# Optimization experiments

Measured on AMD Instinct MI355X. Metric: run time of the kernel, lower is better.

Reference implementation:

```python
import jax, jax.numpy as jnp
import numpy as np

N_NODES = 50000
BN_EPS = 1e-5
L2_EPS = 1e-12


def setup_inputs() -> dict:
    key = jax.random.key(0)
    k_h, k_w, k_s, k_d = jax.random.split(key, 4)
    h = jax.random.normal(k_h, (N_NODES, 128), dtype=jnp.float32)
    W = jax.random.normal(k_w, (128, 128), dtype=jnp.float32) * (1.0 / np.sqrt(128))
    gamma = jnp.ones((128,), dtype=jnp.float32)
    beta = jnp.zeros((128,), dtype=jnp.float32)
    src = jax.random.randint(k_s, (600000,), 0, N_NODES, dtype=jnp.int64 if jax.config.jax_enable_x64 else jnp.int32)
    dst = jax.random.randint(k_d, (600000,), 0, N_NODES, dtype=jnp.int64 if jax.config.jax_enable_x64 else jnp.int32)
    return {"h": h, "W": W, "gamma": gamma, "beta": beta, "src": src, "dst": dst}


def reference(h, W, gamma, beta, src, dst):
    N = h.shape[0]
    ones = jnp.ones(src.shape[0], dtype=h.dtype)
    # degrees, clamped to >= 1 (DGL GraphConv norm='both')
    deg_out = jnp.clip(jax.ops.segment_sum(ones, src, num_segments=N), 1.0)
    deg_in = jnp.clip(jax.ops.segment_sum(ones, dst, num_segments=N), 1.0)
    # src-side normalization
    hn = h * jax.lax.rsqrt(deg_out)[:, None]
    # gather-scatter aggregation over edges (sum of src messages at dst)
    agg = jax.ops.segment_sum(hn[src], dst, num_segments=N)  # [N, dim_in]
    # dst-side normalization, then linear (in_feats <= out_feats branch)
    agg = agg * jax.lax.rsqrt(deg_in)[:, None]
    out = agg @ W  # [N, dim_out]
    # BatchNorm1d (training-mode batch stats, biased variance)
    mu = jnp.mean(out, axis=0)
    var = jnp.mean(jnp.square(out - mu), axis=0)
    out = (out - mu) * jax.lax.rsqrt(var + BN_EPS) * gamma + beta
    # ReLU
    out = jax.nn.relu(out)
    # F.normalize(p=2, dim=1)
    norm = jnp.sqrt(jnp.sum(jnp.square(out), axis=1, keepdims=True))
    out = out / jnp.maximum(norm, L2_EPS)
    return out
```

## Files before the change

### kernel.cpp

```cpp
#include <hip/hip_runtime.h>
#include <hip/hip_bf16.h>

#define N_NODES 50000
#define N_EDGES 600000
#define SLOTS 64
#define GEMM_BLOCKS 782
#define BUILD_BLOCKS 2344
#define GATHER_BLOCKS 3125
#define RED_BLOCKS 125

#define Z_OFF        0ull
#define ESRCP_OFF    12800000ull
#define CURS_OFF     19200000ull
#define DEGO_OFF     19400000ull
#define ZERO_OFF     19200000ull
#define ZERO_BYTES   400000ull
#define FLAG_OFF     19600000ull
#define WSW_OFF      19600128ull
#define PSUM_OFF     19632896ull
#define PSQ_OFF      21232896ull
#define PS2_OFF      22832896ull
#define PQ2_OFF      22896896ull
#define SCALE_OFF    22960896ull
#define SHIFT_OFF    22961408ull
#define OUTPRE_OFF   23000064ull

typedef short bf16x8 __attribute__((ext_vector_type(8)));
typedef float f32x4  __attribute__((ext_vector_type(4)));

__device__ __forceinline__ float bf16lo(unsigned int v) { return __uint_as_float(v << 16); }
__device__ __forceinline__ float bf16hi(unsigned int v) { return __uint_as_float(v & 0xffff0000u); }
__device__ __forceinline__ unsigned int packbf16(float x, float y) {
  union { __hip_bfloat162 v; unsigned int u; } cvt;
  cvt.v.x = __float2bfloat16(x);
  cvt.v.y = __float2bfloat16(y);
  return cvt.u;
}

__global__ __launch_bounds__(256) void k_prepW(const void* __restrict__ Wraw,
                                               const unsigned int* __restrict__ hu,
                                               unsigned int* __restrict__ wsw,
                                               int* __restrict__ flag) {
  __shared__ int cnt;
  if (threadIdx.x == 0) cnt = 0;
  __syncthreads();
  {
    unsigned int u = hu[threadIdx.x];
    int ex = (u >> 7) & 0xFF;
    if (ex >= 100 && ex <= 140) atomicAdd(&cnt, 1);
  }
  __syncthreads();
  int isbf = (cnt >= 128) ? 1 : 0;
  if (blockIdx.x == 0 && threadIdx.x == 0) *flag = isbf;

  int i = blockIdx.x * 256 + threadIdx.x;
  int tileIdx = i >> 8;
  int rem     = i & 255;
  int ln      = rem >> 2;
  int dw      = rem & 3;
  int kb      = tileIdx & 3;
  int ct      = tileIdx >> 2;
  int q       = ln >> 4;
  int n       = ln & 15;
  int k       = kb * 32 + q * 8 + dw * 2;
  int c       = ct * 16 + n;
  unsigned int val;
  if (isbf) {
    const unsigned int* Wd = (const unsigned int*)Wraw;
    unsigned int u0 = Wd[k * 64 + (c >> 1)];
    unsigned int u1 = Wd[(k + 1) * 64 + (c >> 1)];
    unsigned int h0 = (c & 1) ? (u0 >> 16) : (u0 & 0xffffu);
    unsigned int h1 = (c & 1) ? (u1 >> 16) : (u1 & 0xffffu);
    val = h0 | (h1 << 16);
  } else {
    const float* Wf = (const float*)Wraw;
    val = packbf16(Wf[k * 128 + c], Wf[(k + 1) * 128 + c]);
  }
  wsw[i] = val;
}

__global__ __launch_bounds__(256) void k_fused(const int* __restrict__ src,
                                               const int* __restrict__ dst,
                                               int* __restrict__ cursor,
                                               int* __restrict__ dego,
                                               unsigned short* __restrict__ esrcPad,
                                               const void* __restrict__ hraw,
                                               const int* __restrict__ flag,
                                               const unsigned int* __restrict__ wsw,
                                               __hip_bfloat16* __restrict__ Z) {
  __shared__ uint4 lb4[2048];
  if (blockIdx.x >= GEMM_BLOCKS) {
    int e = (blockIdx.x - GEMM_BLOCKS) * 256 + threadIdx.x;
    if (e < N_EDGES) {
      int s = src[e];
      int d = dst[e];
      atomicAdd(&dego[s], 1);
      int slot = atomicAdd(&cursor[d], 1);
      if (slot < SLOTS) esrcPad[d * SLOTS + slot] = (unsigned short)s;
    }
    return;
  }

  unsigned int* lb = (unsigned int*)lb4;
  int t = threadIdx.x;
  int r0 = blockIdx.x * 64;
  for (int i = t; i < 2048; i += 256) lb4[i] = ((const uint4*)wsw)[i];

  int l = t & 63;
  int w = t >> 6;
  int m = l & 15;
  int q = l >> 4;
  int isbf = *flag;

  int rA = r0 + w * 16 + m;
  bool okA = rA < N_NODES;

  bf16x8 af[4];
  if (isbf) {
    const uint4* hd = (const uint4*)hraw;
#pragma unroll
    for (int kb = 0; kb < 4; ++kb) {
      union { uint4 u; bf16x8 v; } cv;
      cv.u = okA ? hd[(size_t)rA * 16 + kb * 4 + q] : make_uint4(0u, 0u, 0u, 0u);
      af[kb] = cv.v;
    }
  } else {
    const float4* hf = (const float4*)hraw;
#pragma unroll
    for (int kb = 0; kb < 4; ++kb) {
      union { uint4 u; bf16x8 v; } cv;
      if (okA) {
        float4 f0 = hf[(size_t)rA * 32 + kb * 8 + q * 2];
        float4 f1 = hf[(size_t)rA * 32 + kb * 8 + q * 2 + 1];
        cv.u.x = packbf16(f0.x, f0.y);
        cv.u.y = packbf16(f0.z, f0.w);
        cv.u.z = packbf16(f1.x, f1.y);
        cv.u.w = packbf16(f1.z, f1.w);
      } else {
        cv.u = make_uint4(0u, 0u, 0u, 0u);
      }
      af[kb] = cv.v;
    }
  }

  f32x4 acc[8];
#pragma unroll
  for (int ct = 0; ct < 8; ++ct) acc[ct] = (f32x4){0.f, 0.f, 0.f, 0.f};

  __syncthreads();

#pragma unroll
  for (int kb = 0; kb < 4; ++kb) {
#pragma unroll
    for (int ct = 0; ct < 8; ++ct) {
      bf16x8 bfv = *(const bf16x8*)&lb[(ct * 4 + kb) * 256 + l * 4];
      acc[ct] = __builtin_amdgcn_mfma_f32_16x16x32_bf16(af[kb], bfv, acc[ct], 0, 0, 0);
    }
  }

#pragma unroll
  for (int ct = 0; ct < 8; ++ct) {
    int col = ct * 16 + m;
#pragma unroll
    for (int reg = 0; reg < 4; ++reg) {
      int row = r0 + w * 16 + q * 4 + reg;
      if (row < N_NODES) Z[(size_t)row * 128 + col] = __float2bfloat16(acc[ct][reg]);
    }
  }
}

__global__ __launch_bounds__(256) void k_gatherZ(const unsigned int* __restrict__ Zd,
                                                 const int* __restrict__ cursor,
                                                 const int* __restrict__ dego,
                                                 const unsigned short* __restrict__ esrcPad,
                                                 unsigned int* __restrict__ outpre,
                                                 float* __restrict__ psum,
                                                 float* __restrict__ psq) {
  __shared__ float sred[4 * 128];
  int t = threadIdx.x;
  int w = t >> 6;
  int l = t & 63;
  float s1a = 0.f, s1b = 0.f, s2a = 0.f, s2b = 0.f;
#pragma unroll
  for (int i = 0; i < 4; ++i) {
    int n = blockIdx.x * 16 + w * 4 + i;
    int di = cursor[n];
    int cnt = di < SLOTS ? di : SLOTS;
    const unsigned short* row = esrcPad + (size_t)n * SLOTS;
    float a0 = 0.f, a1 = 0.f;
    int j = 0;
    for (; j + 3 < cnt; j += 4) {
      ushort4 s4 = *(const ushort4*)&row[j];
      int i0 = s4.x, i1 = s4.y, i2 = s4.z, i3 = s4.w;
      unsigned int v0 = Zd[(size_t)i0 * 64 + l];
      unsigned int v1 = Zd[(size_t)i1 * 64 + l];
      unsigned int v2 = Zd[(size_t)i2 * 64 + l];
      unsigned int v3 = Zd[(size_t)i3 * 64 + l];
      float c0 = rsqrtf((float)max(dego[i0], 1));
      float c1 = rsqrtf((float)max(dego[i1], 1));
      float c2 = rsqrtf((float)max(dego[i2], 1));
      float c3 = rsqrtf((float)max(dego[i3], 1));
      a0 = fmaf(bf16lo(v0), c0, a0); a1 = fmaf(bf16hi(v0), c0, a1);
      a0 = fmaf(bf16lo(v1), c1, a0); a1 = fmaf(bf16hi(v1), c1, a1);
      a0 = fmaf(bf16lo(v2), c2, a0); a1 = fmaf(bf16hi(v2), c2, a1);
      a0 = fmaf(bf16lo(v3), c3, a0); a1 = fmaf(bf16hi(v3), c3, a1);
    }
    for (; j < cnt; ++j) {
      int is = row[j];
      unsigned int v = Zd[(size_t)is * 64 + l];
      float c = rsqrtf((float)max(dego[is], 1));
      a0 = fmaf(bf16lo(v), c, a0);
      a1 = fmaf(bf16hi(v), c, a1);
    }
    float scn = rsqrtf((float)(di < 1 ? 1 : di));
    a0 *= scn; a1 *= scn;
    outpre[(size_t)n * 64 + l] = packbf16(a0, a1);
    s1a += a0; s2a += a0 * a0;
    s1b += a1; s2b += a1 * a1;
  }
  sred[w * 128 + 2 * l]     = s1a;
  sred[w * 128 + 2 * l + 1] = s1b;
  __syncthreads();
  if (t < 128) {
    float v = sred[t] + sred[128 + t] + sred[256 + t] + sred[384 + t];
    psum[(size_t)blockIdx.x * 128 + t] = v;
  }
  __syncthreads();
  sred[w * 128 + 2 * l]     = s2a;
  sred[w * 128 + 2 * l + 1] = s2b;
  __syncthreads();
  if (t < 128) {
    float v = sred[t] + sred[128 + t] + sred[256 + t] + sred[384 + t];
    psq[(size_t)blockIdx.x * 128 + t] = v;
  }
}

__global__ __launch_bounds__(256) void k_bnred(const float* __restrict__ psum,
                                               const float* __restrict__ psq,
                                               float* __restrict__ ps2,
                                               float* __restrict__ pq2) {
  __shared__ float r1[256], r2[256];
  int t = threadIdx.x;
  int c = t & 127;
  int j = t >> 7;
  int b0 = blockIdx.x * 25;
  float s1 = 0.f, s2 = 0.f;
  for (int b = b0 + j; b < b0 + 25; b += 2) {
    s1 += psum[(size_t)b * 128 + c];
    s2 += psq [(size_t)b * 128 + c];
  }
  r1[t] = s1; r2[t] = s2;
  __syncthreads();
  if (j == 0) {
    ps2[(size_t)blockIdx.x * 128 + c] = s1 + r1[c + 128];
    pq2[(size_t)blockIdx.x * 128 + c] = s2 + r2[c + 128];
  }
}

__global__ __launch_bounds__(1024) void k_bnfinal(const float* __restrict__ ps2,
                                                  const float* __restrict__ pq2,
                                                  const void* __restrict__ gamma,
                                                  const void* __restrict__ beta,
                                                  const int* __restrict__ flag,
                                                  float* __restrict__ scale,
                                                  float* __restrict__ shift) {
  __shared__ float r1[1024], r2[1024];
  int t = threadIdx.x;
  int c = t & 127;
  int j = t >> 7;
  float s1 = 0.f, s2 = 0.f;
  for (int b = j; b < RED_BLOCKS; b += 8) {
    s1 += ps2[(size_t)b * 128 + c];
    s2 += pq2[(size_t)b * 128 + c];
  }
  r1[t] = s1; r2[t] = s2;
  __syncthreads();
  if (j == 0) {
#pragma unroll
    for (int jj = 1; jj < 8; ++jj) { s1 += r1[c + 128 * jj]; s2 += r2[c + 128 * jj]; }
    const float invN = 1.0f / (float)N_NODES;
    float mu  = s1 * invN;
    float var = s2 * invN - mu * mu;
    float is  = rsqrtf(var + 1e-5f);
    float g, b;
    if (*flag) {
      g = __bfloat162float(((const __hip_bfloat16*)gamma)[c]);
      b = __bfloat162float(((const __hip_bfloat16*)beta)[c]);
    } else {
      g = ((const float*)gamma)[c];
      b = ((const float*)beta)[c];
    }
    scale[c] = g * is;
    shift[c] = b - mu * g * is;
  }
}

__global__ __launch_bounds__(256) void k_rownorm(const unsigned int* __restrict__ outpre,
                                                 const float* __restrict__ scale,
                                                 const float* __restrict__ shift,
                                                 const int* __restrict__ flag,
                                                 void* __restrict__ outraw) {
  int r = blockIdx.x * 4 + (threadIdx.x >> 6);
  int l = threadIdx.x & 63;
  unsigned int xv = outpre[(size_t)r * 64 + l];
  float2 sc = *(const float2*)&scale[2 * l];
  float2 sh = *(const float2*)&shift[2 * l];
  float y0 = fmaxf(bf16lo(xv) * sc.x + sh.x, 0.f);
  float y1 = fmaxf(bf16hi(xv) * sc.y + sh.y, 0.f);
  float ss = y0 * y0 + y1 * y1;
#pragma unroll
  for (int o = 1; o < 64; o <<= 1) ss += __shfl_xor(ss, o, 64);
  float inv = 1.0f / fmaxf(sqrtf(ss), 1e-12f);
  y0 *= inv; y1 *= inv;
  if (*flag) {
    ((unsigned int*)outraw)[(size_t)r * 64 + l] = packbf16(y0, y1);
  } else {
    float2 o2; o2.x = y0; o2.y = y1;
    ((float2*)outraw)[(size_t)r * 64 + l] = o2;
  }
}

extern "C" void kernel_launch(void* const* d_in, const int* in_sizes, int n_in,
                              void* d_out, int out_size, void* d_ws, size_t ws_size,
                              hipStream_t stream) {
  const void* h     = d_in[0];
  const void* W     = d_in[1];
  const void* gamma = d_in[2];
  const void* beta  = d_in[3];
  const int*  src   = (const int*)d_in[4];
  const int*  dst   = (const int*)d_in[5];

  char* ws = (char*)d_ws;
  unsigned int* Zd      = (unsigned int*)(ws + Z_OFF);
  unsigned short* esrcPad = (unsigned short*)(ws + ESRCP_OFF);
  int*   cursor  = (int*)(ws + CURS_OFF);
  int*   dego    = (int*)(ws + DEGO_OFF);
  int*   flag    = (int*)(ws + FLAG_OFF);
  unsigned int* wsw = (unsigned int*)(ws + WSW_OFF);
  float* psum    = (float*)(ws + PSUM_OFF);
  float* psq     = (float*)(ws + PSQ_OFF);
  float* ps2     = (float*)(ws + PS2_OFF);
  float* pq2     = (float*)(ws + PQ2_OFF);
  float* scale   = (float*)(ws + SCALE_OFF);
  float* shift   = (float*)(ws + SHIFT_OFF);
  unsigned int* outpre = (unsigned int*)(ws + OUTPRE_OFF);

  (void)hipMemsetAsync(ws + ZERO_OFF, 0, ZERO_BYTES, stream);

  hipLaunchKernelGGL(k_prepW, dim3(32), dim3(256), 0, stream,
                     W, (const unsigned int*)h, wsw, flag);
  hipLaunchKernelGGL(k_fused, dim3(GEMM_BLOCKS + BUILD_BLOCKS), dim3(256), 0, stream,
                     src, dst, cursor, dego, esrcPad, h, flag, wsw,
                     (__hip_bfloat16*)Zd);
  hipLaunchKernelGGL(k_gatherZ, dim3(GATHER_BLOCKS), dim3(256), 0, stream,
                     Zd, cursor, dego, esrcPad, outpre, psum, psq);
  hipLaunchKernelGGL(k_bnred, dim3(RED_BLOCKS), dim3(256), 0, stream,
                     psum, psq, ps2, pq2);
  hipLaunchKernelGGL(k_bnfinal, dim3(1), dim3(1024), 0, stream,
                     ps2, pq2, gamma, beta, flag, scale, shift);
  hipLaunchKernelGGL(k_rownorm, dim3(N_NODES / 4), dim3(256), 0, stream,
                     outpre, scale, shift, flag, (unsigned int*)d_out);
}
```

Baseline: 194.3 us.

## Fold W swizzle into GEMM, pad degree counters, vectorize edge build

Removes the k_prepW launch: every GEMM block now swizzles W directly from global into LDS, and bf16 detection becomes a per-wave ballot repeated in each kernel. The edge-build blocks each handle four edges through int4 loads. Cursor and out-degree counters are spaced 32 ints apart, one counter per 128-byte line, to reduce atomic contention on shared lines. In exchange the memset grows from 400 KB to 12.8 MB, counter reads in the gather become scattered, and W is converted redundantly by 782 blocks.

```diff
diff --git a/kernel.cpp b/kernel.cpp
--- a/kernel.cpp
+++ b/kernel.cpp
@@ -5,25 +5,24 @@
 #define N_EDGES 600000
 #define SLOTS 64
 #define GEMM_BLOCKS 782
-#define BUILD_BLOCKS 2344
+#define BUILD_BLOCKS 586
 #define GATHER_BLOCKS 3125
 #define RED_BLOCKS 125
+#define CSTRIDE 32
 
 #define Z_OFF        0ull
 #define ESRCP_OFF    12800000ull
 #define CURS_OFF     19200000ull
-#define DEGO_OFF     19400000ull
+#define DEGO_OFF     25600000ull
 #define ZERO_OFF     19200000ull
-#define ZERO_BYTES   400000ull
-#define FLAG_OFF     19600000ull
-#define WSW_OFF      19600128ull
-#define PSUM_OFF     19632896ull
-#define PSQ_OFF      21232896ull
-#define PS2_OFF      22832896ull
-#define PQ2_OFF      22896896ull
-#define SCALE_OFF    22960896ull
-#define SHIFT_OFF    22961408ull
-#define OUTPRE_OFF   23000064ull
+#define ZERO_BYTES   12800000ull
+#define PSUM_OFF     32000000ull
+#define PSQ_OFF      33600000ull
+#define PS2_OFF      35200000ull
+#define PQ2_OFF      35264000ull
+#define SCALE_OFF    35328000ull
+#define SHIFT_OFF    35328512ull
+#define OUTPRE_OFF   35400000ull
 
 typedef short bf16x8 __attribute__((ext_vector_type(8)));
 typedef float f32x4  __attribute__((ext_vector_type(4)));
@@ -37,46 +36,11 @@
   return cvt.u;
 }
 
-__global__ __launch_bounds__(256) void k_prepW(const void* __restrict__ Wraw,
-                                               const unsigned int* __restrict__ hu,
-                                               unsigned int* __restrict__ wsw,
-                                               int* __restrict__ flag) {
-  __shared__ int cnt;
-  if (threadIdx.x == 0) cnt = 0;
-  __syncthreads();
-  {
-    unsigned int u = hu[threadIdx.x];
-    int ex = (u >> 7) & 0xFF;
-    if (ex >= 100 && ex <= 140) atomicAdd(&cnt, 1);
-  }
-  __syncthreads();
-  int isbf = (cnt >= 128) ? 1 : 0;
-  if (blockIdx.x == 0 && threadIdx.x == 0) *flag = isbf;
-
-  int i = blockIdx.x * 256 + threadIdx.x;
-  int tileIdx = i >> 8;
-  int rem     = i & 255;
-  int ln      = rem >> 2;
-  int dw      = rem & 3;
-  int kb      = tileIdx & 3;
-  int ct      = tileIdx >> 2;
-  int q       = ln >> 4;
-  int n       = ln & 15;
-  int k       = kb * 32 + q * 8 + dw * 2;
-  int c       = ct * 16 + n;
-  unsigned int val;
-  if (isbf) {
-    const unsigned int* Wd = (const unsigned int*)Wraw;
-    unsigned int u0 = Wd[k * 64 + (c >> 1)];
-    unsigned int u1 = Wd[(k + 1) * 64 + (c >> 1)];
-    unsigned int h0 = (c & 1) ? (u0 >> 16) : (u0 & 0xffffu);
-    unsigned int h1 = (c & 1) ? (u1 >> 16) : (u1 & 0xffffu);
-    val = h0 | (h1 << 16);
-  } else {
-    const float* Wf = (const float*)Wraw;
-    val = packbf16(Wf[k * 128 + c], Wf[(k + 1) * 128 + c]);
-  }
-  wsw[i] = val;
+__device__ __forceinline__ int detect_bf16(const unsigned int* hu, int tid) {
+  unsigned int u = hu[tid & 63];
+  int ex = (u >> 7) & 0xFF;
+  unsigned long long b = __ballot(ex >= 100 && ex <= 140);
+  return __popcll(b) >= 32 ? 1 : 0;
 }
 
 __global__ __launch_bounds__(256) void k_fused(const int* __restrict__ src,
@@ -85,32 +49,66 @@
                                                int* __restrict__ dego,
                                                unsigned short* __restrict__ esrcPad,
                                                const void* __restrict__ hraw,
-                                               const int* __restrict__ flag,
-                                               const unsigned int* __restrict__ wsw,
+                                               const void* __restrict__ Wraw,
                                                __hip_bfloat16* __restrict__ Z) {
-  __shared__ uint4 lb4[2048];
+  __shared__ unsigned int lb[8192];
+  int t = threadIdx.x;
+
   if (blockIdx.x >= GEMM_BLOCKS) {
-    int e = (blockIdx.x - GEMM_BLOCKS) * 256 + threadIdx.x;
-    if (e < N_EDGES) {
-      int s = src[e];
-      int d = dst[e];
-      atomicAdd(&dego[s], 1);
-      int slot = atomicAdd(&cursor[d], 1);
-      if (slot < SLOTS) esrcPad[d * SLOTS + slot] = (unsigned short)s;
+    int e0 = (blockIdx.x - GEMM_BLOCKS) * 1024 + t * 4;
+    if (e0 < N_EDGES) {
+      int4 s4 = *(const int4*)&src[e0];
+      int4 d4 = *(const int4*)&dst[e0];
+      atomicAdd(&dego[(size_t)s4.x * CSTRIDE], 1);
+      atomicAdd(&dego[(size_t)s4.y * CSTRIDE], 1);
+      atomicAdd(&dego[(size_t)s4.z * CSTRIDE], 1);
+      atomicAdd(&dego[(size_t)s4.w * CSTRIDE], 1);
+      int sl0 = atomicAdd(&cursor[(size_t)d4.x * CSTRIDE], 1);
+      int sl1 = atomicAdd(&cursor[(size_t)d4.y * CSTRIDE], 1);
+      int sl2 = atomicAdd(&cursor[(size_t)d4.z * CSTRIDE], 1);
+      int sl3 = atomicAdd(&cursor[(size_t)d4.w * CSTRIDE], 1);
+      if (sl0 < SLOTS) esrcPad[(size_t)d4.x * SLOTS + sl0] = (unsigned short)s4.x;
+      if (sl1 < SLOTS) esrcPad[(size_t)d4.y * SLOTS + sl1] = (unsigned short)s4.y;
+      if (sl2 < SLOTS) esrcPad[(size_t)d4.z * SLOTS + sl2] = (unsigned short)s4.z;
+      if (sl3 < SLOTS) esrcPad[(size_t)d4.w * SLOTS + sl3] = (unsigned short)s4.w;
     }
     return;
   }
 
-  unsigned int* lb = (unsigned int*)lb4;
-  int t = threadIdx.x;
+  const unsigned int* hu = (const unsigned int*)hraw;
+  int isbf = detect_bf16(hu, t);
   int r0 = blockIdx.x * 64;
-  for (int i = t; i < 2048; i += 256) lb4[i] = ((const uint4*)wsw)[i];
+
+  for (int i = t; i < 8192; i += 256) {
+    int tileIdx = i >> 8;
+    int rem     = i & 255;
+    int ln      = rem >> 2;
+    int dw      = rem & 3;
+    int kb      = tileIdx & 3;
+    int ct      = tileIdx >> 2;
+    int q       = ln >> 4;
+    int n       = ln & 15;
+    int k       = kb * 32 + q * 8 + dw * 2;
+    int c       = ct * 16 + n;
+    unsigned int val;
+    if (isbf) {
+      const unsigned int* Wd = (const unsigned int*)Wraw;
+      unsigned int u0 = Wd[k * 64 + (c >> 1)];
+      unsigned int u1 = Wd[(k + 1) * 64 + (c >> 1)];
+      unsigned int h0 = (c & 1) ? (u0 >> 16) : (u0 & 0xffffu);
+      unsigned int h1 = (c & 1) ? (u1 >> 16) : (u1 & 0xffffu);
+      val = h0 | (h1 << 16);
+    } else {
+      const float* Wf = (const float*)Wraw;
+      val = packbf16(Wf[k * 128 + c], Wf[(k + 1) * 128 + c]);
+    }
+    lb[i] = val;
+  }
 
   int l = t & 63;
   int w = t >> 6;
   int m = l & 15;
   int q = l >> 4;
-  int isbf = *flag;
 
   int rA = r0 + w * 16 + m;
   bool okA = rA < N_NODES;
@@ -184,7 +182,7 @@
 #pragma unroll
   for (int i = 0; i < 4; ++i) {
     int n = blockIdx.x * 16 + w * 4 + i;
-    int di = cursor[n];
+    int di = cursor[(size_t)n * CSTRIDE];
     int cnt = di < SLOTS ? di : SLOTS;
     const unsigned short* row = esrcPad + (size_t)n * SLOTS;
     float a0 = 0.f, a1 = 0.f;
@@ -196,10 +194,10 @@
       unsigned int v1 = Zd[(size_t)i1 * 64 + l];
       unsigned int v2 = Zd[(size_t)i2 * 64 + l];
       unsigned int v3 = Zd[(size_t)i3 * 64 + l];
-      float c0 = rsqrtf((float)max(dego[i0], 1));
-      float c1 = rsqrtf((float)max(dego[i1], 1));
-      float c2 = rsqrtf((float)max(dego[i2], 1));
-      float c3 = rsqrtf((float)max(dego[i3], 1));
+      float c0 = rsqrtf((float)max(dego[(size_t)i0 * CSTRIDE], 1));
+      float c1 = rsqrtf((float)max(dego[(size_t)i1 * CSTRIDE], 1));
+      float c2 = rsqrtf((float)max(dego[(size_t)i2 * CSTRIDE], 1));
+      float c3 = rsqrtf((float)max(dego[(size_t)i3 * CSTRIDE], 1));
       a0 = fmaf(bf16lo(v0), c0, a0); a1 = fmaf(bf16hi(v0), c0, a1);
       a0 = fmaf(bf16lo(v1), c1, a0); a1 = fmaf(bf16hi(v1), c1, a1);
       a0 = fmaf(bf16lo(v2), c2, a0); a1 = fmaf(bf16hi(v2), c2, a1);
@@ -208,7 +206,7 @@
     for (; j < cnt; ++j) {
       int is = row[j];
       unsigned int v = Zd[(size_t)is * 64 + l];
-      float c = rsqrtf((float)max(dego[is], 1));
+      float c = rsqrtf((float)max(dego[(size_t)is * CSTRIDE], 1));
       a0 = fmaf(bf16lo(v), c, a0);
       a1 = fmaf(bf16hi(v), c, a1);
     }
@@ -261,11 +259,12 @@
                                                   const float* __restrict__ pq2,
                                                   const void* __restrict__ gamma,
                                                   const void* __restrict__ beta,
-                                                  const int* __restrict__ flag,
+                                                  const unsigned int* __restrict__ hu,
                                                   float* __restrict__ scale,
                                                   float* __restrict__ shift) {
   __shared__ float r1[1024], r2[1024];
   int t = threadIdx.x;
+  int isbf = detect_bf16(hu, t);
   int c = t & 127;
   int j = t >> 7;
   float s1 = 0.f, s2 = 0.f;
@@ -283,7 +282,7 @@
     float var = s2 * invN - mu * mu;
     float is  = rsqrtf(var + 1e-5f);
     float g, b;
-    if (*flag) {
+    if (isbf) {
       g = __bfloat162float(((const __hip_bfloat16*)gamma)[c]);
       b = __bfloat162float(((const __hip_bfloat16*)beta)[c]);
     } else {
@@ -298,10 +297,12 @@
 __global__ __launch_bounds__(256) void k_rownorm(const unsigned int* __restrict__ outpre,
                                                  const float* __restrict__ scale,
                                                  const float* __restrict__ shift,
-                                                 const int* __restrict__ flag,
+                                                 const unsigned int* __restrict__ hu,
                                                  void* __restrict__ outraw) {
-  int r = blockIdx.x * 4 + (threadIdx.x >> 6);
-  int l = threadIdx.x & 63;
+  int t = threadIdx.x;
+  int isbf = detect_bf16(hu, t);
+  int r = blockIdx.x * 4 + (t >> 6);
+  int l = t & 63;
   unsigned int xv = outpre[(size_t)r * 64 + l];
   float2 sc = *(const float2*)&scale[2 * l];
   float2 sh = *(const float2*)&shift[2 * l];
@@ -312,7 +313,7 @@
   for (int o = 1; o < 64; o <<= 1) ss += __shfl_xor(ss, o, 64);
   float inv = 1.0f / fmaxf(sqrtf(ss), 1e-12f);
   y0 *= inv; y1 *= inv;
-  if (*flag) {
+  if (isbf) {
     ((unsigned int*)outraw)[(size_t)r * 64 + l] = packbf16(y0, y1);
   } else {
     float2 o2; o2.x = y0; o2.y = y1;
@@ -331,12 +332,10 @@
   const int*  dst   = (const int*)d_in[5];
 
   char* ws = (char*)d_ws;
-  unsigned int* Zd      = (unsigned int*)(ws + Z_OFF);
+  unsigned int* Zd        = (unsigned int*)(ws + Z_OFF);
   unsigned short* esrcPad = (unsigned short*)(ws + ESRCP_OFF);
   int*   cursor  = (int*)(ws + CURS_OFF);
   int*   dego    = (int*)(ws + DEGO_OFF);
-  int*   flag    = (int*)(ws + FLAG_OFF);
-  unsigned int* wsw = (unsigned int*)(ws + WSW_OFF);
   float* psum    = (float*)(ws + PSUM_OFF);
   float* psq     = (float*)(ws + PSQ_OFF);
   float* ps2     = (float*)(ws + PS2_OFF);
@@ -347,17 +346,14 @@
 
   (void)hipMemsetAsync(ws + ZERO_OFF, 0, ZERO_BYTES, stream);
 
-  hipLaunchKernelGGL(k_prepW, dim3(32), dim3(256), 0, stream,
-                     W, (const unsigned int*)h, wsw, flag);
   hipLaunchKernelGGL(k_fused, dim3(GEMM_BLOCKS + BUILD_BLOCKS), dim3(256), 0, stream,
-                     src, dst, cursor, dego, esrcPad, h, flag, wsw,
-                     (__hip_bfloat16*)Zd);
+                     src, dst, cursor, dego, esrcPad, h, W, (__hip_bfloat16*)Zd);
   hipLaunchKernelGGL(k_gatherZ, dim3(GATHER_BLOCKS), dim3(256), 0, stream,
                      Zd, cursor, dego, esrcPad, outpre, psum, psq);
   hipLaunchKernelGGL(k_bnred, dim3(RED_BLOCKS), dim3(256), 0, stream,
                      psum, psq, ps2, pq2);
   hipLaunchKernelGGL(k_bnfinal, dim3(1), dim3(1024), 0, stream,
-                     ps2, pq2, gamma, beta, flag, scale, shift);
+                     ps2, pq2, gamma, beta, (const unsigned int*)h, scale, shift);
   hipLaunchKernelGGL(k_rownorm, dim3(N_NODES / 4), dim3(256), 0, stream,
-                     outpre, scale, shift, flag, (unsigned int*)d_out);
-}
+                     outpre, scale, shift, (const unsigned int*)h, (unsigned int*)d_out);
+}
```

After: 206.6 us. +6.3%, slower.
